# Optimization experiments

Measured on AMD Instinct MI355X. Metric: run time of the kernel, lower is better.

The kernel has to match this reference:

```python
import jax, jax.numpy as jnp
import numpy as np

D_MODEL = 1024
N_HEAD = 16
STRIDE = 1024
SEQ = STRIDE + 1  # time_mask is (stride+1, stride+1) -> N must equal stride+1
BATCH = 4
EPS = 1e-5


def layer_norm(x, g, b):
    mu = jnp.mean(x, axis=-1, keepdims=True)
    var = jnp.var(x, axis=-1, keepdims=True)
    return (x - mu) * jax.lax.rsqrt(var + EPS) * g + b


def quick_gelu(x):
    return x * jax.nn.sigmoid(1.702 * x)


def setup_inputs() -> dict:
    key = jax.random.key(0)
    ks = jax.random.split(key, 12)
    C = D_MODEL
    s = 0.02
    return {
        "x": jax.random.normal(ks[0], (SEQ, BATCH, C), dtype=jnp.float32),
        "qkv_w": jax.random.normal(ks[1], (3 * C, C), dtype=jnp.float32) * s,
        "proj_w": jax.random.normal(ks[2], (C, C), dtype=jnp.float32) * s,
        "proj_b": jnp.zeros((C,), dtype=jnp.float32),
        "ln1_g": jnp.ones((C,), dtype=jnp.float32),
        "ln1_b": jnp.zeros((C,), dtype=jnp.float32),
        "ln2_g": jnp.ones((C,), dtype=jnp.float32),
        "ln2_b": jnp.zeros((C,), dtype=jnp.float32),
        "fc_w": jax.random.normal(ks[3], (4 * C, C), dtype=jnp.float32) * s,
        "fc_b": jnp.zeros((4 * C,), dtype=jnp.float32),
        "cproj_w": jax.random.normal(ks[4], (C, 4 * C), dtype=jnp.float32) * s,
        "cproj_b": jnp.zeros((C,), dtype=jnp.float32),
    }


def _attention(xs, qkv_w, proj_w, proj_b):
    # xs: [N, B, C] (seq-first) -> internal [B, N, C]
    xb = jnp.transpose(xs, (1, 0, 2))
    B, N, C = xb.shape
    H, Dh = N_HEAD, C // N_HEAD
    scale = Dh ** -0.5
    qkv = xb @ qkv_w.T  # [B, N, 3C], no bias (qkv_bias=False)
    qkv = qkv.reshape(B, N, 3, H, Dh).transpose(2, 0, 3, 1, 4)  # [3, B, H, N, Dh]
    q, k, v = qkv[0], qkv[1], qkv[2]
    attn = jnp.einsum("bhnd,bhmd->bhnm", q, k) * scale
    mask = jnp.tril(jnp.ones((N, N), dtype=bool))  # time_mask: causal tril
    attn = jnp.where(mask, attn, -jnp.inf)
    attn = jax.nn.softmax(attn, axis=-1)
    out = jnp.einsum("bhnm,bhmd->bhnd", attn, v)  # [B, H, N, Dh]
    out = out.transpose(0, 2, 1, 3).reshape(B, N, C)
    out = out @ proj_w.T + proj_b
    return jnp.transpose(out, (1, 0, 2)), attn  # back to [N, B, C]


def reference(x, qkv_w, proj_w, proj_b, ln1_g, ln1_b, ln2_g, ln2_b,
              fc_w, fc_b, cproj_w, cproj_b):
    y, attn = _attention(layer_norm(x, ln1_g, ln1_b), qkv_w, proj_w, proj_b)
    x = x + y
    h = layer_norm(x, ln2_g, ln2_b)
    h = quick_gelu(h @ fc_w.T + fc_b) @ cproj_w.T + cproj_b
    x = x + h
    return (x, attn)
```

## Files before the change

### kernel.cpp

```cpp
#include <hip/hip_runtime.h>


typedef unsigned short ushort_t;
typedef __bf16 bf16x8 __attribute__((ext_vector_type(8)));
typedef float f32x4 __attribute__((ext_vector_type(4)));

#define SEQ_N   1025
#define CMODEL  1024
#define NHEAD   16
#define DH      64
#define TTOK    4100
#define MP      4224
#define NPAD    1152
#define BH      64

__device__ __forceinline__ ushort_t f2bf(float f) {
  union { float f; unsigned u; } v; v.f = f;
  unsigned r = v.u + 0x7fffu + ((v.u >> 16) & 1u);
  return (ushort_t)(r >> 16);
}

__device__ __forceinline__ void gl_lds16(const void* g, void* s) {
  __builtin_amdgcn_global_load_lds(
      (const __attribute__((address_space(1))) unsigned int*)g,
      (__attribute__((address_space(3))) unsigned int*)s, 16, 0, 0);
}

__global__ __launch_bounds__(256)
void cvt4(const float* __restrict__ s0, ushort_t* __restrict__ d0,
          const float* __restrict__ s1, ushort_t* __restrict__ d1,
          const float* __restrict__ s2, ushort_t* __restrict__ d2,
          const float* __restrict__ s3, ushort_t* __restrict__ d3) {
  const int b = blockIdx.x;
  const float* s; ushort_t* d; int off;
  if (b < 3072)      { s = s0; d = d0; off = b; }
  else if (b < 4096) { s = s1; d = d1; off = b - 3072; }
  else if (b < 8192) { s = s2; d = d2; off = b - 4096; }
  else               { s = s3; d = d3; off = b - 8192; }
  const int i = (off * 256 + threadIdx.x) * 4;
  const float4 f = *(const float4*)(s + i);
  d[i + 0] = f2bf(f.x);
  d[i + 1] = f2bf(f.y);
  d[i + 2] = f2bf(f.z);
  d[i + 3] = f2bf(f.w);
}

__global__ __launch_bounds__(256)
void ln_bf(const float* __restrict__ xin, const float* __restrict__ g,
           const float* __restrict__ bb, ushort_t* __restrict__ out,
           const float* __restrict__ rbias, float* __restrict__ resout) {
  const int t = blockIdx.x;
  const float* row = xin + (size_t)t * CMODEL;
  const int base = threadIdx.x * 4;
  const float4 v = *(const float4*)(row + base);
  float s = v.x + v.y + v.z + v.w;
  float q = v.x * v.x + v.y * v.y + v.z * v.z + v.w * v.w;
#pragma unroll
  for (int off = 32; off > 0; off >>= 1) {
    s += __shfl_down(s, off);
    q += __shfl_down(q, off);
  }
  __shared__ float sh[8];
  const int wave = threadIdx.x >> 6, lane = threadIdx.x & 63;
  if (lane == 0) { sh[wave] = s; sh[4 + wave] = q; }
  __syncthreads();
  if (threadIdx.x == 0) {
    const float ts = sh[0] + sh[1] + sh[2] + sh[3];
    const float tq = sh[4] + sh[5] + sh[6] + sh[7];
    const float mean = ts * (1.f / CMODEL);
    const float var = tq * (1.f / CMODEL) - mean * mean;
    sh[0] = mean; sh[1] = rsqrtf(var + 1e-5f);
  }
  __syncthreads();
  const float mean = sh[0], rstd = sh[1];
  const float4 gg = *(const float4*)(g + base);
  const float4 bv = *(const float4*)(bb + base);
  ushort_t* orow = out + (size_t)t * CMODEL;
  orow[base + 0] = f2bf((v.x - mean) * rstd * gg.x + bv.x);
  orow[base + 1] = f2bf((v.y - mean) * rstd * gg.y + bv.y);
  orow[base + 2] = f2bf((v.z - mean) * rstd * gg.z + bv.z);
  orow[base + 3] = f2bf((v.w - mean) * rstd * gg.w + bv.w);
  if (resout) {
    const float4 rb = *(const float4*)(rbias + base);
    float4 ro;
    ro.x = v.x + rb.x; ro.y = v.y + rb.y; ro.z = v.z + rb.z; ro.w = v.w + rb.w;
    *(float4*)(resout + (size_t)t * CMODEL + base) = ro;
  }
}

template <int EPI>
__global__ __launch_bounds__(256)
void gemm_bt(const ushort_t* __restrict__ A, int lda,
             const ushort_t* __restrict__ B, int ldb,
             int K,
             const float* __restrict__ bias, const float* __restrict__ res,
             float* __restrict__ outf, ushort_t* __restrict__ outb,
             ushort_t* __restrict__ oq, ushort_t* __restrict__ ok,
             ushort_t* __restrict__ ovt) {
  __shared__ __align__(16) ushort_t lsA[128 * 32];
  __shared__ __align__(16) ushort_t lsB[128 * 32];
  const int tid = threadIdx.x;
  const int wave = tid >> 6, lane = tid & 63;
  const int lr = lane & 15, quad = lane >> 4;
  const int tM = blockIdx.y * 128, tN = blockIdx.x * 128;
  const int kbase = blockIdx.z * K;
  const int waveM = (wave >> 1) * 64, waveN = (wave & 1) * 64;

  f32x4 acc[4][4];
  const f32x4 z4 = {0.f, 0.f, 0.f, 0.f};
#pragma unroll
  for (int i = 0; i < 4; ++i)
#pragma unroll
    for (int j = 0; j < 4; ++j) acc[i][j] = z4;

  for (int k0 = 0; k0 < K; k0 += 32) {
    __syncthreads();
#pragma unroll
    for (int p = 0; p < 2; ++p) {
      const int idx = p * 256 + wave * 64 + lane;
      const int row = idx >> 2, part = idx & 3;
      const int cb = (p * 256 + wave * 64) * 8;
      gl_lds16(A + (size_t)(tM + row) * lda + kbase + k0 + part * 8, lsA + cb);
      gl_lds16(B + (size_t)(tN + row) * ldb + kbase + k0 + part * 8, lsB + cb);
    }
    __syncthreads();
    bf16x8 af[4], bfr[4];
#pragma unroll
    for (int mi = 0; mi < 4; ++mi)
      af[mi] = *(const bf16x8*)(lsA + (waveM + mi * 16 + lr) * 32 + quad * 8);
#pragma unroll
    for (int ni = 0; ni < 4; ++ni)
      bfr[ni] = *(const bf16x8*)(lsB + (waveN + ni * 16 + lr) * 32 + quad * 8);
#pragma unroll
    for (int mi = 0; mi < 4; ++mi)
#pragma unroll
      for (int ni = 0; ni < 4; ++ni)
        acc[mi][ni] = __builtin_amdgcn_mfma_f32_16x16x32_bf16(af[mi], bfr[ni], acc[mi][ni], 0, 0, 0);
  }

#pragma unroll
  for (int mi = 0; mi < 4; ++mi) {
#pragma unroll
    for (int ni = 0; ni < 4; ++ni) {
#pragma unroll
      for (int r = 0; r < 4; ++r) {
        const int m = tM + waveM + mi * 16 + quad * 4 + r;
        const int n = tN + waveN + ni * 16 + lr;
        const float v = acc[mi][ni][r];
        if constexpr (EPI == 0) {
          if (m < TTOK) {
            const int b_ = m & 3, ns = m >> 2;
            const int which = n >> 10, rem = n & 1023, h = rem >> 6, d = rem & 63;
            const int bh = b_ * NHEAD + h;
            const ushort_t bv = f2bf(v);
            if (which == 0)      oq[((size_t)bh * NPAD + ns) * DH + d] = bv;
            else if (which == 1) ok[((size_t)bh * NPAD + ns) * DH + d] = bv;
            else                 ovt[((size_t)bh * DH + d) * NPAD + ns] = bv;
          }
        } else if constexpr (EPI == 3) {
          if (m < TTOK)
            outf[(size_t)m * CMODEL + n] = v + bias[n] + res[(size_t)m * CMODEL + n];
        } else if constexpr (EPI == 4) {
          if (m < TTOK) {
            const float zv = v + bias[n];
            outb[(size_t)m * 4096 + n] = f2bf(zv / (1.f + __expf(-1.702f * zv)));
          }
        } else if constexpr (EPI == 5) {
          if (m < TTOK)
            atomicAdd(outf + (size_t)m * CMODEL + n, v);
        }
      }
    }
  }
}

__global__ __launch_bounds__(256)
void attn_fused(const ushort_t* __restrict__ qb, const ushort_t* __restrict__ kb,
                const ushort_t* __restrict__ vtb, float* __restrict__ attn,
                ushort_t* __restrict__ ao) {
  __shared__ __align__(16) char smem[34816 + 17408 + 512];
  ushort_t* lsK  = (ushort_t*)smem;
  ushort_t* lsP  = (ushort_t*)smem;
  float*    lpart = (float*)smem;
  ushort_t* lsQV = (ushort_t*)(smem + 34816);
  float*    linvs = (float*)(smem + 34816 + 17408);

  const int bh = blockIdx.x;
  const int iT = 8 - blockIdx.y;
  const int tM = iT * 128;
  const int tid = threadIdx.x;
  const int wave = tid >> 6, lane = tid & 63;
  const int lr = lane & 15, quad = lane >> 4;
  const int waveM = (wave >> 1) * 64, waveN = (wave & 1) * 64;

  const ushort_t* Qg = qb + (size_t)bh * NPAD * DH;
  const ushort_t* Kg = kb + (size_t)bh * NPAD * DH;
  const ushort_t* Vg = vtb + (size_t)bh * DH * NPAD;
  float* attn_h = attn + (size_t)bh * ((size_t)SEQ_N * SEQ_N);

#pragma unroll
  for (int p = 0; p < 4; ++p) {
    const int c = p * 256 + wave * 64 + lane;
    const int ks = c >> 9, n = (c >> 2) & 127, part = c & 3;
    gl_lds16(Qg + (size_t)(tM + n) * DH + ks * 32 + part * 8,
             lsQV + (size_t)(p * 256 + wave * 64) * 8);
  }
  __syncthreads();
  bf16x8 aq[4][2];
#pragma unroll
  for (int mi = 0; mi < 4; ++mi)
#pragma unroll
    for (int ks = 0; ks < 2; ++ks)
      aq[mi][ks] = *(const bf16x8*)(lsQV + ks * 4096 + (waveM + mi * 16 + lr) * 32 + quad * 8);
  __syncthreads();

  f32x4 acc[4][4];
  const f32x4 z4 = {0.f, 0.f, 0.f, 0.f};

  float lsum[4][4];
#pragma unroll
  for (int mi = 0; mi < 4; ++mi)
#pragma unroll
    for (int r = 0; r < 4; ++r) lsum[mi][r] = 0.f;

  for (int j = 0; j <= iT; ++j) {
    __syncthreads();
#pragma unroll
    for (int p = 0; p < 4; ++p) {
      const int c = p * 256 + wave * 64 + lane;
      const int ks = c >> 9, n = (c >> 2) & 127, part = c & 3;
      gl_lds16(Kg + (size_t)(j * 128 + n) * DH + ks * 32 + part * 8,
               lsK + (size_t)(p * 256 + wave * 64) * 8);
    }
    __syncthreads();
#pragma unroll
    for (int mi = 0; mi < 4; ++mi)
#pragma unroll
      for (int ni = 0; ni < 4; ++ni) acc[mi][ni] = z4;
    __builtin_amdgcn_s_setprio(1);
#pragma unroll
    for (int ks = 0; ks < 2; ++ks) {
      bf16x8 bk[4];
#pragma unroll
      for (int ni = 0; ni < 4; ++ni)
        bk[ni] = *(const bf16x8*)(lsK + ks * 4096 + (waveN + ni * 16 + lr) * 32 + quad * 8);
#pragma unroll
      for (int mi = 0; mi < 4; ++mi)
#pragma unroll
        for (int ni = 0; ni < 4; ++ni)
          acc[mi][ni] = __builtin_amdgcn_mfma_f32_16x16x32_bf16(aq[mi][ks], bk[ni], acc[mi][ni], 0, 0, 0);
    }
    __builtin_amdgcn_s_setprio(0);
#pragma unroll
    for (int mi = 0; mi < 4; ++mi)
#pragma unroll
      for (int ni = 0; ni < 4; ++ni)
#pragma unroll
        for (int r = 0; r < 4; ++r) {
          const int row = tM + waveM + mi * 16 + quad * 4 + r;
          const int col = j * 128 + waveN + ni * 16 + lr;
          if (col <= row) lsum[mi][r] += __expf(acc[mi][ni][r] * 0.125f);
        }
  }
#pragma unroll
  for (int mi = 0; mi < 4; ++mi)
#pragma unroll
    for (int r = 0; r < 4; ++r) {
      float s = lsum[mi][r];
      s += __shfl_xor(s, 1); s += __shfl_xor(s, 2);
      s += __shfl_xor(s, 4); s += __shfl_xor(s, 8);
      lsum[mi][r] = s;
    }
  __syncthreads();
  if (lr == 0) {
    const int wx = wave & 1;
#pragma unroll
    for (int mi = 0; mi < 4; ++mi)
#pragma unroll
      for (int r = 0; r < 4; ++r)
        lpart[wx * 128 + waveM + mi * 16 + quad * 4 + r] = lsum[mi][r];
  }
  __syncthreads();
  if (tid < 128) linvs[tid] = 1.0f / (lpart[tid] + lpart[128 + tid]);
  __syncthreads();
  float linv[4][4];
#pragma unroll
  for (int mi = 0; mi < 4; ++mi)
#pragma unroll
    for (int r = 0; r < 4; ++r)
      linv[mi][r] = linvs[waveM + mi * 16 + quad * 4 + r];

  f32x4 oacc[2][4];
#pragma unroll
  for (int i = 0; i < 2; ++i)
#pragma unroll
    for (int j = 0; j < 4; ++j) oacc[i][j] = z4;
  const int prow = wave * 32;
  const int wrow = wave * 32;
  const int lcol = lane;

  for (int j = 0; j <= iT; ++j) {
    __syncthreads();
#pragma unroll
    for (int p = 0; p < 4; ++p) {
      const int c = p * 256 + wave * 64 + lane;
      const int ks = c >> 9, n = (c >> 2) & 127, part = c & 3;
      gl_lds16(Kg + (size_t)(j * 128 + n) * DH + ks * 32 + part * 8,
               lsK + (size_t)(p * 256 + wave * 64) * 8);
    }
#pragma unroll
    for (int p = 0; p < 4; ++p) {
      const int c = p * 256 + tid;
      const int n = c >> 4, klc = c & 15;
      const uint4 v = *(const uint4*)(Vg + (size_t)n * NPAD + j * 128 + klc * 8);
      *(uint4*)(lsQV + (size_t)n * 136 + klc * 8) = v;
    }
    __syncthreads();
#pragma unroll
    for (int mi = 0; mi < 4; ++mi)
#pragma unroll
      for (int ni = 0; ni < 4; ++ni) acc[mi][ni] = z4;
    __builtin_amdgcn_s_setprio(1);
#pragma unroll
    for (int ks = 0; ks < 2; ++ks) {
      bf16x8 bk[4];
#pragma unroll
      for (int ni = 0; ni < 4; ++ni)
        bk[ni] = *(const bf16x8*)(lsK + ks * 4096 + (waveN + ni * 16 + lr) * 32 + quad * 8);
#pragma unroll
      for (int mi = 0; mi < 4; ++mi)
#pragma unroll
        for (int ni = 0; ni < 4; ++ni)
          acc[mi][ni] = __builtin_amdgcn_mfma_f32_16x16x32_bf16(aq[mi][ks], bk[ni], acc[mi][ni], 0, 0, 0);
    }
    __builtin_amdgcn_s_setprio(0);
    __syncthreads();
#pragma unroll
    for (int mi = 0; mi < 4; ++mi)
#pragma unroll
      for (int ni = 0; ni < 4; ++ni)
#pragma unroll
        for (int r = 0; r < 4; ++r) {
          const int rowl = waveM + mi * 16 + quad * 4 + r;
          const int coll = waveN + ni * 16 + lr;
          const int row = tM + rowl;
          const int col = j * 128 + coll;
          const float pv = (col <= row) ? __expf(acc[mi][ni][r] * 0.125f) * linv[mi][r] : 0.f;
          lsP[(size_t)rowl * 136 + coll] = f2bf(pv);
        }
    __syncthreads();
    __builtin_amdgcn_s_setprio(1);
#pragma unroll
    for (int ks = 0; ks < 4; ++ks) {
      bf16x8 ap[2], bv[4];
#pragma unroll
      for (int mi2 = 0; mi2 < 2; ++mi2)
        ap[mi2] = *(const bf16x8*)(lsP + (size_t)(prow + mi2 * 16 + lr) * 136 + ks * 32 + quad * 8);
#pragma unroll
      for (int ni = 0; ni < 4; ++ni)
        bv[ni] = *(const bf16x8*)(lsQV + (size_t)(ni * 16 + lr) * 136 + ks * 32 + quad * 8);
#pragma unroll
      for (int mi2 = 0; mi2 < 2; ++mi2)
#pragma unroll
        for (int ni = 0; ni < 4; ++ni)
          oacc[mi2][ni] = __builtin_amdgcn_mfma_f32_16x16x32_bf16(ap[mi2], bv[ni], oacc[mi2][ni], 0, 0, 0);
    }
    __builtin_amdgcn_s_setprio(0);
#pragma unroll 8
    for (int rr = 0; rr < 32; ++rr) {
      const int grow = tM + wrow + rr;
      if (grow >= SEQ_N) break;
      const ushort_t* lrow = lsP + (size_t)(wrow + rr) * 136;
#pragma unroll
      for (int cb = 0; cb < 2; ++cb) {
        const int gcol = j * 128 + cb * 64 + lcol;
        union { unsigned u; float f; } cv;
        cv.u = ((unsigned)lrow[cb * 64 + lcol]) << 16;
        if (gcol < SEQ_N)
          __builtin_nontemporal_store(cv.f, attn_h + (size_t)grow * SEQ_N + gcol);
      }
    }
  }

  const int b_ = bh >> 4, h = bh & 15;
#pragma unroll
  for (int mi2 = 0; mi2 < 2; ++mi2)
#pragma unroll
    for (int ni = 0; ni < 4; ++ni)
#pragma unroll
      for (int r = 0; r < 4; ++r) {
        const int row = tM + prow + mi2 * 16 + quad * 4 + r;
        const int d = ni * 16 + lr;
        if (row < SEQ_N)
          ao[((size_t)row * 4 + b_) * CMODEL + h * DH + d] = f2bf(oacc[mi2][ni][r]);
      }

  const int c0 = tM + 128;
  if (c0 <= 1024) {
    const int width = 1025 - c0;
    for (int r = wave; r < 128; r += 4) {
      float* rp = attn_h + (size_t)(tM + r) * SEQ_N + c0;
      int pre = ((16 - (int)(((uintptr_t)rp) & 15)) >> 2) & 3;
      if (pre > width) pre = width;
      for (int c = lane; c < pre; c += 64) rp[c] = 0.f;
      const int body = (width - pre) >> 2;
      f32x4* bp = (f32x4*)(rp + pre);
      const f32x4 zf4 = {0.f, 0.f, 0.f, 0.f};
      for (int c = lane; c < body; c += 64) __builtin_nontemporal_store(zf4, bp + c);
      for (int c = pre + body * 4 + lane; c < width; c += 64) rp[c] = 0.f;
    }
  }
}

extern "C" void kernel_launch(void* const* d_in, const int* in_sizes, int n_in,
                              void* d_out, int out_size, void* d_ws, size_t ws_size,
                              hipStream_t stream) {
  const float* x       = (const float*)d_in[0];
  const float* qkv_w   = (const float*)d_in[1];
  const float* proj_w  = (const float*)d_in[2];
  const float* proj_b  = (const float*)d_in[3];
  const float* ln1_g   = (const float*)d_in[4];
  const float* ln1_b   = (const float*)d_in[5];
  const float* ln2_g   = (const float*)d_in[6];
  const float* ln2_b   = (const float*)d_in[7];
  const float* fc_w    = (const float*)d_in[8];
  const float* fc_b    = (const float*)d_in[9];
  const float* cproj_w = (const float*)d_in[10];
  const float* cproj_b = (const float*)d_in[11];

  float* out_x = (float*)d_out;
  float* out_attn = out_x + (size_t)TTOK * CMODEL;

  char* p = (char*)d_ws;
  auto alloc = [&](size_t bytes) { char* r = p; p += (bytes + 255) & ~(size_t)255; return r; };
  ushort_t* ln1x  = (ushort_t*)alloc((size_t)MP * CMODEL * 2);
  ushort_t* wqkv  = (ushort_t*)alloc((size_t)3072 * 1024 * 2);
  ushort_t* wproj = (ushort_t*)alloc((size_t)1024 * 1024 * 2);
  ushort_t* wfc   = (ushort_t*)alloc((size_t)4096 * 1024 * 2);
  ushort_t* wcpr  = (ushort_t*)alloc((size_t)1024 * 4096 * 2);
  ushort_t* qb    = (ushort_t*)alloc((size_t)BH * NPAD * DH * 2);
  ushort_t* kb    = (ushort_t*)alloc((size_t)BH * NPAD * DH * 2);
  ushort_t* vtb   = (ushort_t*)alloc((size_t)BH * DH * NPAD * 2);
  ushort_t* aob   = (ushort_t*)alloc((size_t)MP * CMODEL * 2);
  float*    x1    = (float*)alloc((size_t)MP * CMODEL * 4);
  ushort_t* ln2x  = (ushort_t*)alloc((size_t)MP * CMODEL * 2);
  ushort_t* hb    = (ushort_t*)alloc((size_t)MP * 4096 * 2);
  (void)ws_size; (void)in_sizes; (void)n_in; (void)out_size;

  cvt4<<<12288, 256, 0, stream>>>(qkv_w, wqkv, proj_w, wproj, fc_w, wfc, cproj_w, wcpr);

  ln_bf<<<TTOK, 256, 0, stream>>>(x, ln1_g, ln1_b, ln1x, proj_b, x1);

  gemm_bt<0><<<dim3(24, 33, 1), 256, 0, stream>>>(ln1x, 1024, wqkv, 1024, 1024,
      nullptr, nullptr, nullptr, nullptr, qb, kb, vtb);

  attn_fused<<<dim3(64, 9), 256, 0, stream>>>(qb, kb, vtb, out_attn, aob);

  gemm_bt<5><<<dim3(8, 33, 2), 256, 0, stream>>>(aob, 1024, wproj, 1024, 512,
      nullptr, nullptr, x1, nullptr, nullptr, nullptr, nullptr);

  ln_bf<<<TTOK, 256, 0, stream>>>(x1, ln2_g, ln2_b, ln2x, cproj_b, out_x);

  gemm_bt<4><<<dim3(32, 33, 1), 256, 0, stream>>>(ln2x, 1024, wfc, 1024, 1024,
      fc_b, nullptr, nullptr, hb, nullptr, nullptr, nullptr);

  gemm_bt<5><<<dim3(8, 33, 2), 256, 0, stream>>>(hb, 4096, wcpr, 4096, 2048,
      nullptr, nullptr, out_x, nullptr, nullptr, nullptr, nullptr);
}
```

Baseline: 745.6 us.

## Remap workgroup IDs XCD-aware in GEMM and attention; vectorize bf16 stores

Workgroup linear IDs are permuted so that consecutive logical tiles land on the same XCD (lin&7 picks the chiplet), which should improve L2 reuse of shared A/B rows and of the Q/K/V of each head. The attention kernel's remap also changes the order in which causal tiles of different sizes are dispatched. The conversion and layernorm kernels now write four bf16 values with one ushort4 store instead of four scalar stores. The GEMM remap assumes the workgroup count is divisible by 8; if it is not, some tiles would be skipped or duplicated.

New measurement: 743.0 us. About the same (-0.4%).

```diff
diff --git a/kernel.cpp b/kernel.cpp
--- a/kernel.cpp
+++ b/kernel.cpp
@@ -39,10 +39,9 @@
   else               { s = s3; d = d3; off = b - 8192; }
   const int i = (off * 256 + threadIdx.x) * 4;
   const float4 f = *(const float4*)(s + i);
-  d[i + 0] = f2bf(f.x);
-  d[i + 1] = f2bf(f.y);
-  d[i + 2] = f2bf(f.z);
-  d[i + 3] = f2bf(f.w);
+  ushort4 o;
+  o.x = f2bf(f.x); o.y = f2bf(f.y); o.z = f2bf(f.z); o.w = f2bf(f.w);
+  *(ushort4*)(d + i) = o;
 }
 
 __global__ __launch_bounds__(256)
@@ -75,11 +74,12 @@
   const float mean = sh[0], rstd = sh[1];
   const float4 gg = *(const float4*)(g + base);
   const float4 bv = *(const float4*)(bb + base);
-  ushort_t* orow = out + (size_t)t * CMODEL;
-  orow[base + 0] = f2bf((v.x - mean) * rstd * gg.x + bv.x);
-  orow[base + 1] = f2bf((v.y - mean) * rstd * gg.y + bv.y);
-  orow[base + 2] = f2bf((v.z - mean) * rstd * gg.z + bv.z);
-  orow[base + 3] = f2bf((v.w - mean) * rstd * gg.w + bv.w);
+  ushort4 o;
+  o.x = f2bf((v.x - mean) * rstd * gg.x + bv.x);
+  o.y = f2bf((v.y - mean) * rstd * gg.y + bv.y);
+  o.z = f2bf((v.z - mean) * rstd * gg.z + bv.z);
+  o.w = f2bf((v.w - mean) * rstd * gg.w + bv.w);
+  *(ushort4*)(out + (size_t)t * CMODEL + base) = o;
   if (resout) {
     const float4 rb = *(const float4*)(rbias + base);
     float4 ro;
@@ -102,8 +102,18 @@
   const int tid = threadIdx.x;
   const int wave = tid >> 6, lane = tid & 63;
   const int lr = lane & 15, quad = lane >> 4;
-  const int tM = blockIdx.y * 128, tN = blockIdx.x * 128;
-  const int kbase = blockIdx.z * K;
+
+  const int gx = gridDim.x, gy = gridDim.y;
+  const int nwg = gx * gy * gridDim.z;
+  int lin = blockIdx.x + gx * (blockIdx.y + gy * blockIdx.z);
+  lin = (lin & 7) * (nwg >> 3) + (lin >> 3);
+  const int bx = lin % gx;
+  const int byz = lin / gx;
+  const int by = byz % gy;
+  const int bz = byz / gy;
+
+  const int tM = by * 128, tN = bx * 128;
+  const int kbase = bz * K;
   const int waveM = (wave >> 1) * 64, waveN = (wave & 1) * 64;
 
   f32x4 acc[4][4];
@@ -185,8 +195,10 @@
   ushort_t* lsQV = (ushort_t*)(smem + 34816);
   float*    linvs = (float*)(smem + 34816 + 17408);
 
-  const int bh = blockIdx.x;
-  const int iT = 8 - blockIdx.y;
+  int lin = blockIdx.x + 64 * blockIdx.y;
+  lin = (lin & 7) * 72 + (lin >> 3);
+  const int bh = lin / 9;
+  const int iT = 8 - (lin % 9);
   const int tM = iT * 128;
   const int tid = threadIdx.x;
   const int wave = tid >> 6, lane = tid & 63;
```
